# Kernel optimization log

Hardware: AMD Instinct MI355X
Metric: run time of the kernel (lower is better)

The kernel has to match this reference:

```python
import jax, jax.numpy as jnp
import numpy as np

N_NODES = 50000
N_EDGES = 1600000
IN_DIM = 256
HID = 128
BATCH = 16384
EDGE_FEAT = 6
BN_EPS = 1e-5


def _glorot(key, shape):
    fan_in, fan_out = shape[0], shape[1]
    lim = float(np.sqrt(6.0 / (fan_in + fan_out)))
    return jax.random.uniform(key, shape, jnp.float32, -lim, lim)


def setup_inputs() -> dict:
    key = jax.random.key(0)
    ks = jax.random.split(key, 20)
    return {
        "x": jax.random.normal(ks[0], (N_NODES, IN_DIM), jnp.float32),
        "edge_index": jax.random.randint(ks[1], (2, N_EDGES), 0, N_NODES, jnp.int64 if jax.config.jax_enable_x64 else jnp.int32),
        "src_nodes": jax.random.randint(ks[2], (BATCH,), 0, N_NODES),
        "tgt_nodes": jax.random.randint(ks[3], (BATCH,), 0, N_NODES),
        "edge_features": jax.random.uniform(ks[4], (BATCH, EDGE_FEAT), jnp.float32),
        # SAGEConv layer 0: lin_l (aggregated neighbors, has bias), lin_r (root, no bias)
        "sage_wl0": _glorot(ks[5], (IN_DIM, HID)),
        "sage_b0": jnp.zeros((HID,), jnp.float32),
        "sage_wr0": _glorot(ks[6], (IN_DIM, HID)),
        # SAGEConv layer 1
        "sage_wl1": _glorot(ks[7], (HID, HID)),
        "sage_b1": jnp.zeros((HID,), jnp.float32),
        "sage_wr1": _glorot(ks[8], (HID, HID)),
        # edge_processor: Linear(6, 64)
        "ep_w": _glorot(ks[9], (EDGE_FEAT, HID // 2)),
        "ep_b": jnp.zeros((HID // 2,), jnp.float32),
        # predictor: Linear(320,128) -> ReLU -> BN(128) -> Linear(128,64) -> ReLU -> Linear(64,1) -> Sigmoid
        "p1_w": _glorot(ks[10], (2 * HID + HID // 2, HID)),
        "p1_b": jnp.zeros((HID,), jnp.float32),
        "bn_gamma": jnp.ones((HID,), jnp.float32),
        "bn_beta": jnp.zeros((HID,), jnp.float32),
        "bn_mean": jnp.zeros((HID,), jnp.float32),
        "bn_var": jnp.ones((HID,), jnp.float32),
        "p2_w": _glorot(ks[11], (HID, HID // 2)),
        "p2_b": jnp.zeros((HID // 2,), jnp.float32),
        "p3_w": _glorot(ks[12], (HID // 2, 1)),
        "p3_b": jnp.zeros((1,), jnp.float32),
    }


def _sage_conv(h, src, dst, w_l, b, w_r):
    # PyG SAGEConv(mean): out_i = W_l @ mean_{j in N(i)} h_j + b + W_r @ h_i
    n = h.shape[0]
    agg = jax.ops.segment_sum(h[src], dst, num_segments=n)  # [N, d]
    deg = jax.ops.segment_sum(jnp.ones((src.shape[0],), h.dtype), dst, num_segments=n)
    mean = agg / jnp.maximum(deg, 1.0)[:, None]
    return mean @ w_l + b + h @ w_r


def reference(x, edge_index, src_nodes, tgt_nodes, edge_features,
              sage_wl0, sage_b0, sage_wr0, sage_wl1, sage_b1, sage_wr1,
              ep_w, ep_b, p1_w, p1_b, bn_gamma, bn_beta, bn_mean, bn_var,
              p2_w, p2_b, p3_w, p3_b):
    src, dst = edge_index[0], edge_index[1]
    h = _sage_conv(x, src, dst, sage_wl0, sage_b0, sage_wr0)
    h = jax.nn.relu(h)  # dropout is identity in eval mode
    h = _sage_conv(h, src, dst, sage_wl1, sage_b1, sage_wr1)
    src_emb = h[src_nodes]  # [B, HID]
    tgt_emb = h[tgt_nodes]  # [B, HID]
    edge_proc = jax.nn.relu(edge_features @ ep_w + ep_b)  # [B, HID//2]
    combined = jnp.concatenate([src_emb, tgt_emb, edge_proc], axis=1)  # [B, 320]
    z = jax.nn.relu(combined @ p1_w + p1_b)
    z = (z - bn_mean) / jnp.sqrt(bn_var + BN_EPS) * bn_gamma + bn_beta  # BN eval mode
    z = jax.nn.relu(z @ p2_w + p2_b)
    return jax.nn.sigmoid(z @ p3_w + p3_b)  # [B, 1]
```

## Files before the change

### kernel.cpp

```cpp
#include <hip/hip_runtime.h>
#include <hip/hip_bf16.h>

#define N_NODES 50000
#define N_EDGES 1600000
#define BATCH   16384
#define HID     128
#define NBUCK   782
#define NBLK    1000
#define EPB     1600

using short8  = __attribute__((ext_vector_type(8))) short;
using floatx4 = __attribute__((ext_vector_type(4))) float;
using floatv4 = __attribute__((ext_vector_type(4))) float;
using uint2v  = __attribute__((ext_vector_type(2))) unsigned;
using uintx4  = __attribute__((ext_vector_type(4))) unsigned;
typedef unsigned short ushort_t;

__device__ __forceinline__ float bflo(unsigned u){ return __uint_as_float(u << 16); }
__device__ __forceinline__ float bfhi(unsigned u){ return __uint_as_float(u & 0xffff0000u); }
__device__ __forceinline__ float bf1(ushort_t u){ return __uint_as_float(((unsigned)u) << 16); }
__device__ __forceinline__ ushort_t f2bf(float f){
    unsigned u = __float_as_uint(f);
    return (ushort_t)((u + 0x7fffu + ((u >> 16) & 1u)) >> 16);
}
__device__ __forceinline__ int geti(const void* p, long long i, int is64){
    return is64 ? (int)((const long long*)p)[i] : ((const int*)p)[i];
}

__global__ void k_detect(const unsigned* __restrict__ xbits,
                         const unsigned* __restrict__ eibits, int* flags){
    if (threadIdx.x == 0 && blockIdx.x == 0){
        int big = 0;
        for (int i = 0; i < 256; ++i){
            unsigned u = xbits[i];
            unsigned e0 = (u >> 7)  & 0xFF;
            unsigned e1 = (u >> 23) & 0xFF;
            if (e0 >= 140) big++;
            if (e1 >= 140) big++;
        }
        flags[0] = (big > 0) ? 1 : 0;
        int oddnz = 0;
        for (int i = 0; i < 256; ++i)
            if (eibits[2*i + 1] != 0) oddnz++;
        flags[1] = (oddnz == 0) ? 1 : 0;
    }
}

#define NT 19
struct ConvDesc { const void* src[NT]; int cum[NT + 1]; };
__global__ void k_conv(ConvDesc d, ushort_t* __restrict__ dst, const int* __restrict__ flags){
    int i = blockIdx.x*256 + threadIdx.x;
    if (i >= d.cum[NT]) return;
    int seg = 0;
    while (i >= d.cum[seg + 1]) seg++;
    int off = i - d.cum[seg];
    ushort_t v;
    if (flags[0]) v = f2bf(((const float*)d.src[seg])[off]);
    else          v = ((const ushort_t*)d.src[seg])[off];
    dst[i] = v;
}

#define OFF_WL0 0
#define OFF_WR0 32768
#define OFF_WL1 65536
#define OFF_WR1 81920
#define OFF_B0  98304
#define OFF_B1  98432
#define OFF_EPW 98560
#define OFF_EPB 98944
#define OFF_P1W 99008
#define OFF_P1B 139968
#define OFF_BNG 140096
#define OFF_BNB 140224
#define OFF_BNM 140352
#define OFF_BNV 140480
#define OFF_P2W 140608
#define OFF_P2B 148800
#define OFF_P3W 148864
#define OFF_EF  148928
#define OFF_P3B 247232
#define CW_TOT  247233

#define PACK_TOT 147584
__global__ void k_pack(const ushort_t* __restrict__ cw,
                       ushort_t* __restrict__ bp0, ushort_t* __restrict__ bp1,
                       ushort_t* __restrict__ bpp1, ushort_t* __restrict__ bpp2,
                       float* __restrict__ bnf){
    int i = blockIdx.x*256 + threadIdx.x;
    if (i < 65536){
        int j = i & 7, lane = (i >> 3) & 63, c = (i >> 9) & 15, kk = i >> 13;
        int k = kk*32 + (lane >> 4)*8 + j;
        int n = c*16 + (lane & 15);
        bp0[i] = (n < 128) ? cw[OFF_WL0 + k*128 + n] : cw[OFF_WR0 + k*128 + (n-128)];
    } else if (i < 98304){
        int i2 = i - 65536;
        int j = i2 & 7, lane = (i2 >> 3) & 63, c = (i2 >> 9) & 15, kk = i2 >> 13;
        int k = kk*32 + (lane >> 4)*8 + j;
        int n = c*16 + (lane & 15);
        bp1[i2] = (n < 128) ? cw[OFF_WL1 + k*128 + n] : cw[OFF_WR1 + k*128 + (n-128)];
    } else if (i < 139264){
        int i2 = i - 98304;
        int j = i2 & 7, lane = (i2 >> 3) & 63, ct = (i2 >> 9) & 7, kk = i2 >> 12;
        int k = kk*32 + (lane >> 4)*8 + j;
        int n = ct*16 + (lane & 15);
        bpp1[i2] = cw[OFF_P1W + k*128 + n];
    } else if (i < 147456){
        int i2 = i - 139264;
        int j = i2 & 7, lane = (i2 >> 3) & 63, ct = (i2 >> 9) & 3, kk = i2 >> 11;
        int k = kk*32 + (lane >> 4)*8 + j;
        int n = ct*16 + (lane & 15);
        bpp2[i2] = cw[OFF_P2W + k*64 + n];
    } else if (i < PACK_TOT){
        int n = i - 147456;
        float g = bf1(cw[OFF_BNG + n]), b = bf1(cw[OFF_BNB + n]);
        float m = bf1(cw[OFF_BNM + n]), v = bf1(cw[OFF_BNV + n]);
        float sc = g / sqrtf(v + 1e-5f);
        bnf[n] = sc; bnf[128 + n] = b - m*sc;
    }
}

__global__ __launch_bounds__(256)
void k_xcast(const float* __restrict__ x, ushort_t* __restrict__ xbf,
             const int* __restrict__ flags){
    if (!flags[0]) return;
    int i = blockIdx.x*256 + threadIdx.x;
    floatv4 v = ((const floatv4*)x)[i];
    uint2v o;
    o.x = (unsigned)f2bf(v[0]) | ((unsigned)f2bf(v[1]) << 16);
    o.y = (unsigned)f2bf(v[2]) | ((unsigned)f2bf(v[3]) << 16);
    ((uint2v*)xbf)[i] = o;
}

__global__ __launch_bounds__(256)
void kb_hist(const void* __restrict__ ei, int* __restrict__ hist,
             const int* __restrict__ flags){
    __shared__ int lh[NBUCK];
    for (int i = threadIdx.x; i < NBUCK; i += 256) lh[i] = 0;
    __syncthreads();
    int i64 = flags[1];
    int e0 = blockIdx.x * EPB;
    for (int e = e0 + threadIdx.x; e < e0 + EPB; e += 256){
        int d = geti(ei, (long long)N_EDGES + e, i64);
        atomicAdd(&lh[d >> 6], 1);
    }
    __syncthreads();
    for (int i = threadIdx.x; i < NBUCK; i += 256)
        hist[i * NBLK + blockIdx.x] = lh[i];
}

__global__ __launch_bounds__(1024)
void kb_scancol(int* __restrict__ hist, int* __restrict__ btot){
    __shared__ int sh[1024];
    int b = blockIdx.x, t = threadIdx.x;
    int v = (t < NBLK) ? hist[b*NBLK + t] : 0;
    sh[t] = v; __syncthreads();
    for (int o = 1; o < 1024; o <<= 1){
        int x = (t >= o) ? sh[t-o] : 0;
        __syncthreads();
        sh[t] += x;
        __syncthreads();
    }
    if (t < NBLK) hist[b*NBLK + t] = sh[t] - v;
    if (t == 1023) btot[b] = sh[1023];
}

__global__ __launch_bounds__(1024)
void kb_scanbase(const int* __restrict__ btot, int* __restrict__ bbase,
                 int* __restrict__ off){
    __shared__ int sh[1024];
    int t = threadIdx.x;
    int v = (t < NBUCK) ? btot[t] : 0;
    sh[t] = v; __syncthreads();
    for (int o = 1; o < 1024; o <<= 1){
        int x = (t >= o) ? sh[t-o] : 0;
        __syncthreads();
        sh[t] += x;
        __syncthreads();
    }
    if (t < NBUCK) bbase[t] = sh[t] - v;
    if (t == 0){ bbase[NBUCK] = N_EDGES; off[N_NODES] = N_EDGES; }
}

__global__ __launch_bounds__(256)
void kb_scatter(const void* __restrict__ ei, const int* __restrict__ hist,
                const int* __restrict__ bbase, unsigned* __restrict__ ebuf,
                const int* __restrict__ flags){
    __shared__ int lcur[NBUCK];
    for (int i = threadIdx.x; i < NBUCK; i += 256)
        lcur[i] = bbase[i] + hist[i*NBLK + blockIdx.x];
    __syncthreads();
    int i64 = flags[1];
    int e0 = blockIdx.x * EPB;
    for (int e = e0 + threadIdx.x; e < e0 + EPB; e += 256){
        int s = geti(ei, e, i64);
        int d = geti(ei, (long long)N_EDGES + e, i64);
        int p = atomicAdd(&lcur[d >> 6], 1);
        ebuf[p] = (unsigned)s | ((unsigned)(d & 63) << 16);
    }
}

__global__ __launch_bounds__(256)
void kb_csr(const unsigned* __restrict__ ebuf, const int* __restrict__ bbase,
            ushort_t* __restrict__ csr, int* __restrict__ off){
    __shared__ int ldeg[64];
    int b = blockIdx.x, t = threadIdx.x;
    int ebase = bbase[b], eend = bbase[b+1];
    if (t < 64) ldeg[t] = 0;
    __syncthreads();
    for (int i = ebase + t; i < eend; i += 256)
        atomicAdd(&ldeg[(ebuf[i] >> 16) & 63], 1);
    __syncthreads();
    if (t < 64){
        int v = ldeg[t];
        int sum = v;
        #pragma unroll
        for (int o = 1; o < 64; o <<= 1){
            int x = __shfl_up(sum, o, 64);
            if (t >= o) sum += x;
        }
        int excl = sum - v;
        int node = b*64 + t;
        if (node < N_NODES) off[node] = ebase + excl;
        ldeg[t] = excl;
    }
    __syncthreads();
    for (int i = ebase + t; i < eend; i += 256){
        unsigned u = ebuf[i];
        int p = atomicAdd(&ldeg[(u >> 16) & 63], 1);
        csr[ebase + p] = (ushort_t)(u & 0xffffu);
    }
}

template<int KSTEPS, bool MF32>
__global__ __launch_bounds__(256)
void k_gemm2(const void* __restrict__ a_raw, const ushort_t* __restrict__ a_bf,
             const ushort_t* __restrict__ Bp, ushort_t* __restrict__ out,
             int M, const int* __restrict__ flags)
{
    const int lane = threadIdx.x & 63;
    const int w    = threadIdx.x >> 6;
    const int l16  = lane & 15;
    const int q    = lane >> 4;
    const int S    = KSTEPS * 32;
    const int m_base = blockIdx.x * 64;

    const ushort_t* A = (MF32 && flags[0]) ? a_bf : (const ushort_t*)a_raw;

    const ushort_t* arow[4];
    bool ok[4];
    #pragma unroll
    for (int rt = 0; rt < 4; ++rt){
        int m = m_base + rt*16 + l16;
        ok[rt] = (m < M);
        arow[rt] = A + (size_t)(ok[rt] ? m : 0) * S + q*8;
    }
    const short8* bbase = (const short8*)(Bp + (size_t)(w*4)*64*8) + lane;

    floatx4 acc[4][4] = {};
    for (int kk = 0; kk < KSTEPS; ++kk){
        short8 b[4];
        #pragma unroll
        for (int ci = 0; ci < 4; ++ci)
            b[ci] = bbase[(kk*16 + ci)*64];
        short8 a[4];
        #pragma unroll
        for (int rt = 0; rt < 4; ++rt){
            short8 af = {0,0,0,0,0,0,0,0};
            if (ok[rt]) af = *(const short8*)(arow[rt] + kk*32);
            a[rt] = af;
        }
        #pragma unroll
        for (int rt = 0; rt < 4; ++rt)
            #pragma unroll
            for (int ci = 0; ci < 4; ++ci)
                acc[rt][ci] = __builtin_amdgcn_mfma_f32_16x16x32_bf16(a[rt], b[ci], acc[rt][ci], 0, 0, 0);
    }

    #pragma unroll
    for (int rt = 0; rt < 4; ++rt){
        int row_b = m_base + rt*16 + q*4;
        #pragma unroll
        for (int r = 0; r < 4; ++r){
            int row = row_b + r;
            if (row < M){
                #pragma unroll
                for (int ci = 0; ci < 4; ++ci)
                    out[(size_t)row*256 + w*64 + ci*16 + l16] = f2bf(acc[rt][ci][r]);
            }
        }
    }
}

__global__ __launch_bounds__(256)
void k_agg(const int* __restrict__ off, const ushort_t* __restrict__ csr,
           const ushort_t* __restrict__ yr, const ushort_t* __restrict__ bias,
           ushort_t* __restrict__ out, int do_relu)
{
    int v = blockIdx.x*4 + (threadIdx.x >> 6);
    if (v >= N_NODES) return;
    const int l = threadIdx.x & 63;
    const int g = l >> 4;
    const int c = l & 15;
    int e0 = off[v], e1 = off[v+1];

    float a0=0,a1=0,a2=0,a3=0,a4=0,a5=0,a6=0,a7=0;
    int p = e0;
    for (; p + 4 <= e1; p += 4){
        int u = csr[p + g];
        uintx4 d = *(const uintx4*)(yr + (size_t)u*256 + c*8);
        a0 += bflo(d.x); a1 += bfhi(d.x);
        a2 += bflo(d.y); a3 += bfhi(d.y);
        a4 += bflo(d.z); a5 += bfhi(d.z);
        a6 += bflo(d.w); a7 += bfhi(d.w);
    }
    if (p + g < e1){
        int u = csr[p + g];
        uintx4 d = *(const uintx4*)(yr + (size_t)u*256 + c*8);
        a0 += bflo(d.x); a1 += bfhi(d.x);
        a2 += bflo(d.y); a3 += bfhi(d.y);
        a4 += bflo(d.z); a5 += bfhi(d.z);
        a6 += bflo(d.w); a7 += bfhi(d.w);
    }
    #pragma unroll
    for (int m = 16; m <= 32; m <<= 1){
        a0 += __shfl_xor(a0, m, 64); a1 += __shfl_xor(a1, m, 64);
        a2 += __shfl_xor(a2, m, 64); a3 += __shfl_xor(a3, m, 64);
        a4 += __shfl_xor(a4, m, 64); a5 += __shfl_xor(a5, m, 64);
        a6 += __shfl_xor(a6, m, 64); a7 += __shfl_xor(a7, m, 64);
    }
    if (g == 0){
        float inv = 1.f / (float)max(e1 - e0, 1);
        uintx4 rr = *(const uintx4*)(yr + (size_t)v*256 + 128 + c*8);
        uintx4 bb = *(const uintx4*)(bias + c*8);
        float v0 = a0*inv + bflo(rr.x) + bflo(bb.x);
        float v1 = a1*inv + bfhi(rr.x) + bfhi(bb.x);
        float v2 = a2*inv + bflo(rr.y) + bflo(bb.y);
        float v3 = a3*inv + bfhi(rr.y) + bfhi(bb.y);
        float v4 = a4*inv + bflo(rr.z) + bflo(bb.z);
        float v5 = a5*inv + bfhi(rr.z) + bfhi(bb.z);
        float v6 = a6*inv + bflo(rr.w) + bflo(bb.w);
        float v7 = a7*inv + bfhi(rr.w) + bfhi(bb.w);
        if (do_relu){
            v0=fmaxf(v0,0.f); v1=fmaxf(v1,0.f); v2=fmaxf(v2,0.f); v3=fmaxf(v3,0.f);
            v4=fmaxf(v4,0.f); v5=fmaxf(v5,0.f); v6=fmaxf(v6,0.f); v7=fmaxf(v7,0.f);
        }
        uintx4 o;
        o.x = (unsigned)f2bf(v0) | ((unsigned)f2bf(v1) << 16);
        o.y = (unsigned)f2bf(v2) | ((unsigned)f2bf(v3) << 16);
        o.z = (unsigned)f2bf(v4) | ((unsigned)f2bf(v5) << 16);
        o.w = (unsigned)f2bf(v6) | ((unsigned)f2bf(v7) << 16);
        *(uintx4*)(out + (size_t)v*128 + c*8) = o;
    }
}

__global__ __launch_bounds__(256)
void k_pred2(const ushort_t* __restrict__ h2,
             const void* __restrict__ srcn, const void* __restrict__ tgtn,
             const ushort_t* __restrict__ cw, const ushort_t* __restrict__ bpp1,
             const ushort_t* __restrict__ bpp2, const float* __restrict__ bnf,
             void* __restrict__ outp, const int* __restrict__ flags)
{
    __shared__ ushort_t comb[64][328];
    __shared__ ushort_t zbuf[64][136];
    __shared__ ushort_t z2buf[64][68];
    __shared__ float    partial[4][64];
    __shared__ int      sid[64], tid_[64];

    const int t    = threadIdx.x;
    const int lane = t & 63;
    const int w    = t >> 6;
    const int l16  = lane & 15;
    const int q    = lane >> 4;
    const int row0 = blockIdx.x * 64;
    const int i64  = flags[1];

    if (t < 64){ sid[t] = geti(srcn, row0 + t, i64); tid_[t] = geti(tgtn, row0 + t, i64); }
    __syncthreads();

    const unsigned* h2u = (const unsigned*)h2;
    #pragma unroll 4
    for (int r = w*16; r < w*16 + 16; ++r){
        unsigned us = h2u[(size_t)sid[r]*64 + lane];
        unsigned ut = h2u[(size_t)tid_[r]*64 + lane];
        *(unsigned*)&comb[r][2*lane]       = us;
        *(unsigned*)&comb[r][128 + 2*lane] = ut;
    }
    {
        int r = t >> 2, c0 = (t & 3) * 16;
        float efv[6];
        #pragma unroll
        for (int k = 0; k < 6; ++k) efv[k] = bf1(cw[OFF_EF + (row0 + r)*6 + k]);
        #pragma unroll
        for (int c = 0; c < 16; ++c){
            int n = c0 + c;
            float a = bf1(cw[OFF_EPB + n]);
            #pragma unroll
            for (int k = 0; k < 6; ++k) a += efv[k] * bf1(cw[OFF_EPW + k*64 + n]);
            comb[r][256 + n] = f2bf(fmaxf(a, 0.f));
        }
    }
    __syncthreads();

    floatx4 acc[4][2] = {};
    for (int kk = 0; kk < 10; ++kk){
        short8 a[4];
        #pragma unroll
        for (int rt = 0; rt < 4; ++rt)
            a[rt] = *(const short8*)&comb[rt*16 + l16][kk*32 + q*8];
        #pragma unroll
        for (int ci = 0; ci < 2; ++ci){
            short8 b = *(const short8*)&bpp1[(((kk*8) + (w*2 + ci))*64 + lane)*8];
            #pragma unroll
            for (int rt = 0; rt < 4; ++rt)
                acc[rt][ci] = __builtin_amdgcn_mfma_f32_16x16x32_bf16(a[rt], b, acc[rt][ci], 0, 0, 0);
        }
    }
    #pragma unroll
    for (int ci = 0; ci < 2; ++ci){
        int n = w*32 + ci*16 + l16;
        float b1v = bf1(cw[OFF_P1B + n]);
        float sc = bnf[n], sh = bnf[128 + n];
        #pragma unroll
        for (int rt = 0; rt < 4; ++rt)
            #pragma unroll
            for (int r = 0; r < 4; ++r){
                float v = fmaxf(acc[rt][ci][r] + b1v, 0.f) * sc + sh;
                zbuf[rt*16 + q*4 + r][n] = f2bf(v);
            }
    }
    __syncthreads();

    floatx4 acc2[4] = {};
    for (int kk = 0; kk < 4; ++kk){
        short8 b = *(const short8*)&bpp2[(((kk*4) + w)*64 + lane)*8];
        #pragma unroll
        for (int rt = 0; rt < 4; ++rt){
            short8 a = *(const short8*)&zbuf[rt*16 + l16][kk*32 + q*8];
            acc2[rt] = __builtin_amdgcn_mfma_f32_16x16x32_bf16(a, b, acc2[rt], 0, 0, 0);
        }
    }
    {
        int n = w*16 + l16;
        float b2v = bf1(cw[OFF_P2B + n]);
        #pragma unroll
        for (int rt = 0; rt < 4; ++rt)
            #pragma unroll
            for (int r = 0; r < 4; ++r)
                z2buf[rt*16 + q*4 + r][n] = f2bf(fmaxf(acc2[rt][r] + b2v, 0.f));
    }
    __syncthreads();

    {
        int r = t & 63, seg = t >> 6;
        float s = 0.f;
        #pragma unroll
        for (int c = 0; c < 16; ++c){
            int n = seg*16 + c;
            s += bf1(z2buf[r][n]) * bf1(cw[OFF_P3W + n]);
        }
        partial[seg][r] = s;
    }
    __syncthreads();
    if (t < 64){
        float zf = partial[0][t] + partial[1][t] + partial[2][t] + partial[3][t] + bf1(cw[OFF_P3B]);
        float sg = 1.f / (1.f + __expf(-zf));
        if (flags[0]) ((float*)outp)[row0 + t] = sg;
        else          ((ushort_t*)outp)[row0 + t] = f2bf(sg);
    }
}

extern "C" void kernel_launch(void* const* d_in, const int* in_sizes, int n_in,
                              void* d_out, int out_size, void* d_ws, size_t ws_size,
                              hipStream_t stream)
{
    const void* x    = d_in[0];
    const void* ei   = d_in[1];
    const void* srcn = d_in[2];
    const void* tgtn = d_in[3];

    char* p = (char*)d_ws;
    auto carve = [&](size_t bytes)->char*{ char* r = p; p += (bytes + 511) & ~size_t(511); return r; };
    int* flags = (int*)carve(64);
    int* off   = (int*)carve((N_NODES+1)*4);
    int* btot  = (int*)carve(NBUCK*4);
    int* bbase = (int*)carve((NBUCK+1)*4);
    ushort_t* csr = (ushort_t*)carve((size_t)N_EDGES*2);
    ushort_t* yr  = (ushort_t*)carve((size_t)N_NODES*256*2);
    ushort_t* h   = (ushort_t*)carve((size_t)N_NODES*128*2);
    ushort_t* cw  = (ushort_t*)carve((size_t)CW_TOT*2);
    ushort_t* bp0 = (ushort_t*)carve((size_t)65536*2);
    ushort_t* bp1 = (ushort_t*)carve((size_t)32768*2);
    ushort_t* bpp1= (ushort_t*)carve((size_t)40960*2);
    ushort_t* bpp2= (ushort_t*)carve((size_t)8192*2);
    float*    bnf = (float*)carve(256*4);
    ushort_t* xbf = (ushort_t*)carve((size_t)N_NODES*256*2);

    int*      hist = (int*)yr;
    unsigned* ebuf = (unsigned*)((char*)yr + 8u*1024*1024);

    k_detect<<<1, 64, 0, stream>>>((const unsigned*)x, (const unsigned*)ei, flags);

    ConvDesc cd;
    const int srcidx[NT] = {5,7,8,10,6,9,11,12,13,14,15,16,17,18,19,20,21,4,22};
    const int lens[NT]   = {32768,32768,16384,16384,128,128,384,64,40960,128,128,128,128,128,8192,64,64,98304,1};
    int run = 0;
    for (int i = 0; i < NT; ++i){ cd.src[i] = d_in[srcidx[i]]; cd.cum[i] = run; run += lens[i]; }
    cd.cum[NT] = run;
    k_conv<<<(CW_TOT+255)/256, 256, 0, stream>>>(cd, cw, flags);
    k_pack<<<(PACK_TOT+255)/256, 256, 0, stream>>>(cw, bp0, bp1, bpp1, bpp2, bnf);
    k_xcast<<<12500, 256, 0, stream>>>((const float*)x, xbf, flags);

    kb_hist    <<<NBLK, 256, 0, stream>>>(ei, hist, flags);
    kb_scancol <<<NBUCK, 1024, 0, stream>>>(hist, btot);
    kb_scanbase<<<1, 1024, 0, stream>>>(btot, bbase, off);
    kb_scatter <<<NBLK, 256, 0, stream>>>(ei, hist, bbase, ebuf, flags);
    kb_csr     <<<NBUCK, 256, 0, stream>>>(ebuf, bbase, csr, off);

    int gblocks = (N_NODES + 63) / 64;
    k_gemm2<8, true ><<<gblocks, 256, 0, stream>>>(x, xbf, bp0, yr, N_NODES, flags);
    k_agg<<<(N_NODES+3)/4, 256, 0, stream>>>(off, csr, yr, cw+OFF_B0, h, 1);
    k_gemm2<4, false><<<gblocks, 256, 0, stream>>>(h, nullptr, bp1, yr, N_NODES, flags);
    k_agg<<<(N_NODES+3)/4, 256, 0, stream>>>(off, csr, yr, cw+OFF_B1, h, 0);

    k_pred2<<<BATCH/64, 256, 0, stream>>>(h, srcn, tgtn, cw, bpp1, bpp2, bnf, d_out, flags);
}
```

Measured before the change: 388.2 us.

## Parallelize detect kernel, shrink bucket-sort block count, dual-accumulate gather in aggregation

The single-thread flag-detection loop becomes a 256-thread kernel that combines its checks with shared-memory atomicOr. The bucket sort now uses 256 blocks of 6250 edges instead of 1000 blocks of 1600, so the column scan can run with 256 threads and fewer scan steps. The aggregation kernel processes 8 neighbors per iteration with two independent accumulator sets, putting more loads in flight per wave. The trade-offs are fewer blocks for histogram and scatter, with more serial work and shared-memory atomics per block, and higher register use in aggregation.

```diff
diff --git a/kernel.cpp b/kernel.cpp
--- a/kernel.cpp
+++ b/kernel.cpp
@@ -6,8 +6,8 @@
 #define BATCH   16384
 #define HID     128
 #define NBUCK   782
-#define NBLK    1000
-#define EPB     1600
+#define NBLK    256
+#define EPB     6250
 
 using short8  = __attribute__((ext_vector_type(8))) short;
 using floatx4 = __attribute__((ext_vector_type(4))) float;
@@ -29,21 +29,17 @@
 
 __global__ void k_detect(const unsigned* __restrict__ xbits,
                          const unsigned* __restrict__ eibits, int* flags){
-    if (threadIdx.x == 0 && blockIdx.x == 0){
-        int big = 0;
-        for (int i = 0; i < 256; ++i){
-            unsigned u = xbits[i];
-            unsigned e0 = (u >> 7)  & 0xFF;
-            unsigned e1 = (u >> 23) & 0xFF;
-            if (e0 >= 140) big++;
-            if (e1 >= 140) big++;
-        }
-        flags[0] = (big > 0) ? 1 : 0;
-        int oddnz = 0;
-        for (int i = 0; i < 256; ++i)
-            if (eibits[2*i + 1] != 0) oddnz++;
-        flags[1] = (oddnz == 0) ? 1 : 0;
-    }
+    __shared__ int f[2];
+    int t = threadIdx.x;
+    if (t < 2) f[t] = 0;
+    __syncthreads();
+    unsigned u = xbits[t];
+    unsigned e0 = (u >> 7)  & 0xFF;
+    unsigned e1 = (u >> 23) & 0xFF;
+    if (e0 >= 140 || e1 >= 140) atomicOr(&f[0], 1);
+    if (eibits[2*t + 1] != 0)   atomicOr(&f[1], 1);
+    __syncthreads();
+    if (t == 0){ flags[0] = f[0]; flags[1] = f[1] ? 0 : 1; }
 }
 
 #define NT 19
@@ -148,20 +144,20 @@
         hist[i * NBLK + blockIdx.x] = lh[i];
 }
 
-__global__ __launch_bounds__(1024)
+__global__ __launch_bounds__(256)
 void kb_scancol(int* __restrict__ hist, int* __restrict__ btot){
-    __shared__ int sh[1024];
+    __shared__ int sh[256];
     int b = blockIdx.x, t = threadIdx.x;
-    int v = (t < NBLK) ? hist[b*NBLK + t] : 0;
+    int v = hist[b*NBLK + t];
     sh[t] = v; __syncthreads();
-    for (int o = 1; o < 1024; o <<= 1){
+    for (int o = 1; o < 256; o <<= 1){
         int x = (t >= o) ? sh[t-o] : 0;
         __syncthreads();
         sh[t] += x;
         __syncthreads();
     }
-    if (t < NBLK) hist[b*NBLK + t] = sh[t] - v;
-    if (t == 1023) btot[b] = sh[1023];
+    hist[b*NBLK + t] = sh[t] - v;
+    if (t == 255) btot[b] = sh[255];
 }
 
 __global__ __launch_bounds__(1024)
@@ -302,25 +298,44 @@
     const int g = l >> 4;
     const int c = l & 15;
     int e0 = off[v], e1 = off[v+1];
+    const ushort_t* yb = yr + c*8;
 
     float a0=0,a1=0,a2=0,a3=0,a4=0,a5=0,a6=0,a7=0;
+    float b0=0,b1=0,b2=0,b3=0,b4=0,b5=0,b6=0,b7=0;
     int p = e0;
-    for (; p + 4 <= e1; p += 4){
-        int u = csr[p + g];
-        uintx4 d = *(const uintx4*)(yr + (size_t)u*256 + c*8);
-        a0 += bflo(d.x); a1 += bfhi(d.x);
-        a2 += bflo(d.y); a3 += bfhi(d.y);
-        a4 += bflo(d.z); a5 += bfhi(d.z);
-        a6 += bflo(d.w); a7 += bfhi(d.w);
+    for (; p + 8 <= e1; p += 8){
+        int uA = csr[p + g];
+        int uB = csr[p + 4 + g];
+        uintx4 dA = *(const uintx4*)(yb + (size_t)uA*256);
+        uintx4 dB = *(const uintx4*)(yb + (size_t)uB*256);
+        a0 += bflo(dA.x); a1 += bfhi(dA.x);
+        a2 += bflo(dA.y); a3 += bfhi(dA.y);
+        a4 += bflo(dA.z); a5 += bfhi(dA.z);
+        a6 += bflo(dA.w); a7 += bfhi(dA.w);
+        b0 += bflo(dB.x); b1 += bfhi(dB.x);
+        b2 += bflo(dB.y); b3 += bfhi(dB.y);
+        b4 += bflo(dB.z); b5 += bfhi(dB.z);
+        b6 += bflo(dB.w); b7 += bfhi(dB.w);
+    }
+    if (p + 4 <= e1){
+        int uA = csr[p + g];
+        uintx4 dA = *(const uintx4*)(yb + (size_t)uA*256);
+        a0 += bflo(dA.x); a1 += bfhi(dA.x);
+        a2 += bflo(dA.y); a3 += bfhi(dA.y);
+        a4 += bflo(dA.z); a5 += bfhi(dA.z);
+        a6 += bflo(dA.w); a7 += bfhi(dA.w);
+        p += 4;
     }
     if (p + g < e1){
-        int u = csr[p + g];
-        uintx4 d = *(const uintx4*)(yr + (size_t)u*256 + c*8);
-        a0 += bflo(d.x); a1 += bfhi(d.x);
-        a2 += bflo(d.y); a3 += bfhi(d.y);
-        a4 += bflo(d.z); a5 += bfhi(d.z);
-        a6 += bflo(d.w); a7 += bfhi(d.w);
-    }
+        int uB = csr[p + g];
+        uintx4 dB = *(const uintx4*)(yb + (size_t)uB*256);
+        b0 += bflo(dB.x); b1 += bfhi(dB.x);
+        b2 += bflo(dB.y); b3 += bfhi(dB.y);
+        b4 += bflo(dB.z); b5 += bfhi(dB.z);
+        b6 += bflo(dB.w); b7 += bfhi(dB.w);
+    }
+    a0 += b0; a1 += b1; a2 += b2; a3 += b3;
+    a4 += b4; a5 += b5; a6 += b6; a7 += b7;
     #pragma unroll
     for (int m = 16; m <= 32; m <<= 1){
         a0 += __shfl_xor(a0, m, 64); a1 += __shfl_xor(a1, m, 64);
@@ -498,7 +513,7 @@
     int*      hist = (int*)yr;
     unsigned* ebuf = (unsigned*)((char*)yr + 8u*1024*1024);
 
-    k_detect<<<1, 64, 0, stream>>>((const unsigned*)x, (const unsigned*)ei, flags);
+    k_detect<<<1, 256, 0, stream>>>((const unsigned*)x, (const unsigned*)ei, flags);
 
     ConvDesc cd;
     const int srcidx[NT] = {5,7,8,10,6,9,11,12,13,14,15,16,17,18,19,20,21,4,22};
@@ -511,7 +526,7 @@
     k_xcast<<<12500, 256, 0, stream>>>((const float*)x, xbf, flags);
 
     kb_hist    <<<NBLK, 256, 0, stream>>>(ei, hist, flags);
-    kb_scancol <<<NBUCK, 1024, 0, stream>>>(hist, btot);
+    kb_scancol <<<NBUCK, 256, 0, stream>>>(hist, btot);
     kb_scanbase<<<1, 1024, 0, stream>>>(btot, bbase, off);
     kb_scatter <<<NBLK, 256, 0, stream>>>(ei, hist, bbase, ebuf, flags);
     kb_csr     <<<NBUCK, 256, 0, stream>>>(ebuf, bbase, csr, off);
```

Result: faster. 348.6 us (-10.2%).
